# Performance work log

Measured on AMD Instinct MI355X. Metric: run time of the kernel, lower is better.

## Reference

```python
import jax, jax.numpy as jnp
import numpy as np

N = 50000
E = 800000
IN_DIM = 128
HID = 128
HEADS = 8
OUT_DIM = 64
NEG_SLOPE = 0.2


def setup_inputs() -> dict:
    key = jax.random.key(0)
    ks = jax.random.split(key, 10)
    x = jax.random.normal(ks[0], (N, IN_DIM), dtype=jnp.float32)
    edge_index = jax.random.randint(ks[1], (2, E), 0, N, dtype=jnp.int64)
    c1 = HID // HEADS  # 16 per-head channels, layer 1
    # layer 1 params (GATConv: lin has no bias; att_src/att_dst are [1,H,C])
    W1 = jax.random.normal(ks[2], (IN_DIM, HEADS * c1), dtype=jnp.float32) * 0.1
    att_src1 = jax.random.normal(ks[3], (1, HEADS, c1), dtype=jnp.float32) * 0.1
    att_dst1 = jax.random.normal(ks[4], (1, HEADS, c1), dtype=jnp.float32) * 0.1
    b1 = jnp.zeros((HEADS * c1,), dtype=jnp.float32)  # concat=True -> bias size H*C
    # layer 2 params (heads=1, concat=False)
    W2 = jax.random.normal(ks[5], (HID, OUT_DIM), dtype=jnp.float32) * 0.1
    att_src2 = jax.random.normal(ks[6], (1, 1, OUT_DIM), dtype=jnp.float32) * 0.1
    att_dst2 = jax.random.normal(ks[7], (1, 1, OUT_DIM), dtype=jnp.float32) * 0.1
    b2 = jnp.zeros((OUT_DIM,), dtype=jnp.float32)
    return {"x": x, "edge_index": edge_index,
            "W1": W1, "att_src1": att_src1, "att_dst1": att_dst1, "b1": b1,
            "W2": W2, "att_src2": att_src2, "att_dst2": att_dst2, "b2": b2}


def _gat_conv(x, src, dst, W, att_src, att_dst, bias, heads, concat):
    n = x.shape[0]
    c = W.shape[1] // heads
    h = (x @ W).reshape(n, heads, c)                      # [N,H,C]
    a_src = jnp.sum(h * att_src, axis=-1)                 # [N,H]
    a_dst = jnp.sum(h * att_dst, axis=-1)                 # [N,H]
    e = a_src[src] + a_dst[dst]                           # [E,H]
    e = jnp.where(e > 0, e, NEG_SLOPE * e)                # leaky_relu
    # segment softmax over incoming edges of each dst node
    m = jax.ops.segment_max(e, dst, num_segments=n)       # [N,H]
    ex = jnp.exp(e - m[dst])
    denom = jax.ops.segment_sum(ex, dst, num_segments=n)  # [N,H]
    alpha = ex / (denom[dst] + 1e-16)                     # [E,H]
    msg = h[src] * alpha[:, :, None]                      # [E,H,C]
    out = jax.ops.segment_sum(msg, dst, num_segments=n)   # [N,H,C]
    out = out.reshape(n, heads * c) if concat else out.mean(axis=1)
    return out + bias


def reference(x, edge_index, W1, att_src1, att_dst1, b1, W2, att_src2, att_dst2, b2):
    # add self-loops (PyG GATConv default add_self_loops=True)
    loops = jnp.arange(N, dtype=edge_index.dtype)
    src = jnp.concatenate([edge_index[0], loops])
    dst = jnp.concatenate([edge_index[1], loops])
    h = _gat_conv(x, src, dst, W1, att_src1, att_dst1, b1, HEADS, True)
    h = jax.nn.elu(h)
    out = _gat_conv(h, src, dst, W2, att_src2, att_dst2, b2, 1, False)
    return jax.nn.log_softmax(out, axis=1)
```

## Files before the change

kernel.cpp:

```cpp
#include <hip/hip_runtime.h>
#include <math.h>

#define N_NODES 50000
#define E_EDGES 800000
#define ET      (E_EDGES + N_NODES)
#define IN_DIM  128
#define HID     128
#define HEADS   8
#define C1      16
#define OUT_DIM 64
#define NEG_SLOPE 0.2f
#define LOG2E   1.4426950408889634f

#define TILE    8192
#define NT      ((ET + TILE - 1) / TILE)
#define NB      ((N_NODES + 255) / 256)

#define CONV_BLOCKS (N_NODES * IN_DIM / 4 / 256)
#define PREP_BLOCKS 112
#define MEGA_A (NT + CONV_BLOCKS + PREP_BLOCKS)
#define L1T_BLOCKS ((N_NODES + 63) / 64)
#define L1TA 391
#define L1TB (L1T_BLOCKS - L1TA)
#define FUSE_BLOCKS ((N_NODES + 15) / 16)

typedef unsigned int uint32;
typedef __attribute__((ext_vector_type(8))) short bf16x8;
typedef __attribute__((ext_vector_type(4))) float f32x4;
typedef __attribute__((ext_vector_type(2))) float f32x2;

static __device__ __forceinline__ unsigned short f2bf(float f) {
    uint32 u = __float_as_uint(f);
    u += 0x7FFFu + ((u >> 16) & 1u);
    return (unsigned short)(u >> 16);
}

static __device__ __forceinline__ unsigned char f2fp8(float f) {
    int pk = __builtin_amdgcn_cvt_pk_fp8_f32(f, f, 0, false);
    return (unsigned char)(pk & 0xFF);
}


__global__ __launch_bounds__(256) void prep_all(
        const int* __restrict__ dst, int* __restrict__ cnt,
        const float* __restrict__ x, unsigned short* __restrict__ xb,
        const float* __restrict__ W1, const float* __restrict__ as1,
        const float* __restrict__ ad1, const float* __restrict__ W2,
        const float* __restrict__ as2, const float* __restrict__ ad2,
        unsigned short* __restrict__ w1t, unsigned short* __restrict__ p1t,
        unsigned short* __restrict__ w2t, unsigned short* __restrict__ p2t) {
    __shared__ int hist[NB];
    int blk = blockIdx.x, t = threadIdx.x;
    if (blk < NT) {
        for (int b = t; b < NB; b += 256) hist[b] = 0;
        __syncthreads();
        int base = blk * TILE;
        #pragma unroll
        for (int it = 0; it < TILE / 256; ++it) {
            int i = base + it * 256 + t;
            if (i < ET) {
                int d = (i < E_EDGES) ? dst[i] : (i - E_EDGES);
                atomicAdd(&hist[d >> 8], 1);
            }
        }
        __syncthreads();
        for (int b = t; b < NB; b += 256) cnt[blk * NB + b] = hist[b];
    } else if (blk < NT + CONV_BLOCKS) {
        int i = (blk - NT) * 256 + t;
        float4 v = ((const float4*)x)[i];
        ushort4 o;
        o.x = f2bf(v.x); o.y = f2bf(v.y); o.z = f2bf(v.z); o.w = f2bf(v.w);
        ((ushort4*)xb)[i] = o;
    } else {
        int b = blk - NT - CONV_BLOCKS;
        if (b < 64) {
            int i = b * 256 + t;
            int n = i >> 7, k = i & 127;
            w1t[n * IN_DIM + k] = f2bf(W1[k * HID + n]);
        } else if (b < 96) {
            int i = (b - 64) * 256 + t;
            int n = i >> 7, k = i & 127;
            w2t[n * HID + k] = f2bf(W2[k * OUT_DIM + n]);
        } else if (b < 104) {
            int i = (b - 96) * 256 + t;
            int j = i >> 7, k = i & 127;
            int hh = j & 7;
            const float* a = (j < 8) ? as1 : ad1;
            float acc = 0.f;
            #pragma unroll
            for (int c = 0; c < C1; ++c)
                acc = fmaf(W1[k * HID + hh * C1 + c], a[hh * C1 + c], acc);
            p1t[j * IN_DIM + k] = f2bf(acc * LOG2E);
        } else {
            int i = (b - 104) * 256 + t;
            int j = i >> 7, k = i & 127;
            if (j < 2) {
                const float* a = (j == 0) ? as2 : ad2;
                float acc = 0.f;
                #pragma unroll
                for (int c = 0; c < OUT_DIM; ++c)
                    acc = fmaf(W2[k * OUT_DIM + c], a[c], acc);
                p2t[j * HID + k] = f2bf(acc * LOG2E);
            } else {
                p2t[j * HID + k] = 0;
            }
        }
    }
}


static __device__ __forceinline__ void l1_transform_body(
        int bb, int t,
        const unsigned short* __restrict__ xb, const unsigned short* __restrict__ w1t,
        const unsigned short* __restrict__ p1t, unsigned char* __restrict__ h1f,
        float* __restrict__ a_src, float* __restrict__ a_dst) {
    int w = t >> 6, lane = t & 63;
    int l15 = lane & 15, quad = lane >> 4;
    int n0 = bb * 64 + w * 16;
    int mrow = n0 + l15;
    int mload = (mrow < N_NODES) ? mrow : (N_NODES - 1);

    bf16x8 af[4];
    #pragma unroll
    for (int s = 0; s < 4; ++s)
        af[s] = *(const bf16x8*)&xb[(size_t)mload * IN_DIM + s * 32 + quad * 8];

    #pragma unroll
    for (int tt = 0; tt < 9; ++tt) {
        const unsigned short* Brow = (tt < 8) ? &w1t[(tt * 16 + l15) * IN_DIM]
                                              : &p1t[l15 * IN_DIM];
        f32x4 acc = {0.f, 0.f, 0.f, 0.f};
        #pragma unroll
        for (int s = 0; s < 4; ++s) {
            bf16x8 bf = *(const bf16x8*)&Brow[s * 32 + quad * 8];
            acc = __builtin_amdgcn_mfma_f32_16x16x32_bf16(af[s], bf, acc, 0, 0, 0);
        }
        int nodeb = n0 + quad * 4;
        if (tt < 8) {
            int ch = tt * 16 + l15;
            #pragma unroll
            for (int r = 0; r < 4; ++r)
                if (nodeb + r < N_NODES)
                    h1f[(size_t)(nodeb + r) * HID + ch] = f2fp8(acc[r]);
        } else {
            #pragma unroll
            for (int r = 0; r < 4; ++r) {
                if (nodeb + r < N_NODES) {
                    if (l15 < 8) a_src[(nodeb + r) * HEADS + l15] = acc[r];
                    else         a_dst[(nodeb + r) * HEADS + (l15 - 8)] = acc[r];
                }
            }
        }
    }
}


__global__ __launch_bounds__(256) void scatter_l1ta(
        const int* __restrict__ src, const int* __restrict__ dst,
        const int* __restrict__ cnt, int* __restrict__ bucketStart,
        uint32* __restrict__ pairs,
        const unsigned short* __restrict__ xb, const unsigned short* __restrict__ w1t,
        const unsigned short* __restrict__ p1t, unsigned char* __restrict__ h1f,
        float* __restrict__ a_src, float* __restrict__ a_dst) {
    __shared__ int lcur[NB];
    __shared__ int sscan[256];
    int t = threadIdx.x;
    if (blockIdx.x >= NT) {
        l1_transform_body(blockIdx.x - NT, t, xb, w1t, p1t, h1f, a_src, a_dst);
        return;
    }
    int tile = blockIdx.x;

    int run = 0, total = 0;
    if (t < NB) {
        for (int k = 0; k < NT; ++k) {
            int c = cnt[k * NB + t];
            if (k < tile) run += c;
            total += c;
        }
    }
    sscan[t] = (t < NB) ? total : 0;
    __syncthreads();
    #pragma unroll
    for (int off = 1; off < 256; off <<= 1) {
        int add = (t >= off) ? sscan[t - off] : 0;
        __syncthreads();
        sscan[t] += add;
        __syncthreads();
    }
    int bstart = sscan[t] - total;
    if (t < NB) {
        lcur[t] = bstart + run;
        if (tile == 0) bucketStart[t] = bstart;
    }
    if (tile == 0 && t == 0) bucketStart[NB] = ET;
    __syncthreads();

    int base = tile * TILE;
    #pragma unroll
    for (int it = 0; it < TILE / 256; ++it) {
        int i = base + it * 256 + t;
        if (i < ET) {
            int s, d;
            if (i < E_EDGES) { s = src[i]; d = dst[i]; }
            else             { s = d = i - E_EDGES; }
            int pos = atomicAdd(&lcur[d >> 8], 1);
            pairs[pos] = ((uint32)s << 8) | (uint32)(d & 255);
        }
    }
}


__global__ __launch_bounds__(256) void bucket_l1tb(
        const uint32* __restrict__ pairs, const int* __restrict__ bucketStart,
        int* __restrict__ row_start, int* __restrict__ csr_src,
        const unsigned short* __restrict__ xb, const unsigned short* __restrict__ w1t,
        const unsigned short* __restrict__ p1t, unsigned char* __restrict__ h1f,
        float* __restrict__ a_src, float* __restrict__ a_dst) {
    __shared__ int sdeg[256];
    __shared__ int sscan[256];
    int t = threadIdx.x;
    if (blockIdx.x >= NB) {
        l1_transform_body(blockIdx.x - NB + L1TA, t, xb, w1t, p1t, h1f, a_src, a_dst);
        return;
    }
    int b = blockIdx.x;
    int beg = bucketStart[b], end = bucketStart[b + 1];
    sdeg[t] = 0;
    __syncthreads();
    for (int j = beg + t; j < end; j += 256)
        atomicAdd(&sdeg[pairs[j] & 255u], 1);
    __syncthreads();
    int v = sdeg[t];
    sscan[t] = v;
    __syncthreads();
    #pragma unroll
    for (int off = 1; off < 256; off <<= 1) {
        int add = (t >= off) ? sscan[t - off] : 0;
        __syncthreads();
        sscan[t] += add;
        __syncthreads();
    }
    int pos0 = beg + sscan[t] - v;
    int n = b * 256 + t;
    if (n < N_NODES) row_start[n] = pos0;
    if (b == 0 && t == 0) row_start[N_NODES] = ET;
    __syncthreads();
    sscan[t] = pos0;
    __syncthreads();
    for (int j = beg + t; j < end; j += 256) {
        uint32 p = pairs[j];
        int pos = atomicAdd(&sscan[p & 255u], 1);
        csr_src[pos] = (int)(p >> 8);
    }
}


__global__ __launch_bounds__(256) void l1agg_l2t(
        const unsigned char* __restrict__ h1f, const float* __restrict__ a_src,
        const float* __restrict__ a_dst, const int* __restrict__ row_start,
        const int* __restrict__ csr_src, const float* __restrict__ b1,
        const unsigned short* __restrict__ w2t, const unsigned short* __restrict__ p2t,
        unsigned char* __restrict__ h2f, float* __restrict__ a_src2,
        float* __restrict__ a_dst2) {
    __shared__ unsigned short ha[16][128];
    __shared__ int sdeg16[16];
    __shared__ unsigned char perm[16];
    int t = threadIdx.x;
    int w = t >> 6;
    uint32 lane = t & 63;
    uint32 quarter = lane >> 4;
    uint32 lane16 = lane & 15;
    int n0blk = blockIdx.x * 16;

    if (t < 16) {
        int n = n0blk + t;
        int nc = (n < N_NODES) ? n : (N_NODES - 1);
        sdeg16[t] = row_start[nc + 1] - row_start[nc];
    }
    __syncthreads();
    if (t < 16) {
        int d = sdeg16[t];
        int r = 0;
        #pragma unroll
        for (int j = 0; j < 16; ++j) {
            int dj = sdeg16[j];
            r += (dj < d) || (dj == d && j < t);
        }
        perm[r] = (unsigned char)t;
    }
    __syncthreads();

    {
        uint32 c0 = lane16 * 8u;
        uint32 h = lane16 >> 1;
        int n_local = (int)perm[w * 4 + (int)quarter];
        int n = n0blk + n_local;
        int nc = (n < N_NODES) ? n : (N_NODES - 1);
        int beg = row_start[nc], end = row_start[nc + 1];
        int cnt = end - beg;
        int kmax = cnt;
        kmax = max(kmax, __shfl_xor(kmax, 16, 64));
        kmax = max(kmax, __shfl_xor(kmax, 32, 64));
        float adst = a_dst[nc * HEADS + h];
        float l = 0.f;
        float a0 = 0.f, a1 = 0.f, a2 = 0.f, a3 = 0.f;
        float a4 = 0.f, a5 = 0.f, a6 = 0.f, a7 = 0.f;

        auto edge = [&](float e0, uint2 u0, bool live) {
            float e = e0 + adst;
            e = fmaxf(e, NEG_SLOPE * e);
            e = live ? e : -10000.f;
            float p = exp2f(e);
            l += p;
            f32x2 f01 = __builtin_amdgcn_cvt_pk_f32_fp8((int)u0.x, false);
            f32x2 f23 = __builtin_amdgcn_cvt_pk_f32_fp8((int)u0.x, true);
            f32x2 f45 = __builtin_amdgcn_cvt_pk_f32_fp8((int)u0.y, false);
            f32x2 f67 = __builtin_amdgcn_cvt_pk_f32_fp8((int)u0.y, true);
            a0 = fmaf(p, f01[0], a0);
            a1 = fmaf(p, f01[1], a1);
            a2 = fmaf(p, f23[0], a2);
            a3 = fmaf(p, f23[1], a3);
            a4 = fmaf(p, f45[0], a4);
            a5 = fmaf(p, f45[1], a5);
            a6 = fmaf(p, f67[0], a6);
            a7 = fmaf(p, f67[1], a7);
        };

        int k = 0;
        uint32 ssn[8];
        if (k + 8 <= kmax) {
            #pragma unroll
            for (int q = 0; q < 8; ++q) {
                int j = beg + q;
                int jc = (j < end) ? j : (end - 1);
                ssn[q] = (uint32)csr_src[jc];
            }
        }
        for (; k + 8 <= kmax; k += 8) {
            uint32 ss[8]; float ee[8]; uint2 uu[8];
            #pragma unroll
            for (int q = 0; q < 8; ++q) ss[q] = ssn[q];
            #pragma unroll
            for (int q = 0; q < 8; ++q) ee[q] = a_src[ss[q] * 8u + h];
            #pragma unroll
            for (int q = 0; q < 8; ++q) uu[q] = *(const uint2*)&h1f[(ss[q] << 7) + c0];
            int kn = k + 8;
            if (kn + 8 <= kmax) {
                #pragma unroll
                for (int q = 0; q < 8; ++q) {
                    int j = beg + kn + q;
                    int jc = (j < end) ? j : (end - 1);
                    ssn[q] = (uint32)csr_src[jc];
                }
            }
            #pragma unroll
            for (int q = 0; q < 8; ++q) edge(ee[q], uu[q], k + q < cnt);
        }
        for (; k < kmax; k += 4) {
            uint32 ss[4]; float ee[4]; uint2 uu[4];
            #pragma unroll
            for (int q = 0; q < 4; ++q) {
                int j = beg + k + q;
                int jc = (j < end) ? j : (end - 1);
                ss[q] = (uint32)csr_src[jc];
            }
            #pragma unroll
            for (int q = 0; q < 4; ++q) ee[q] = a_src[ss[q] * 8u + h];
            #pragma unroll
            for (int q = 0; q < 4; ++q) uu[q] = *(const uint2*)&h1f[(ss[q] << 7) + c0];
            #pragma unroll
            for (int q = 0; q < 4; ++q) edge(ee[q], uu[q], k + q < cnt);
        }

        float inv = 1.f / (l + 1e-16f);
        float v0 = a0 * inv + b1[c0 + 0];
        float v1 = a1 * inv + b1[c0 + 1];
        float v2 = a2 * inv + b1[c0 + 2];
        float v3 = a3 * inv + b1[c0 + 3];
        float v4 = a4 * inv + b1[c0 + 4];
        float v5 = a5 * inv + b1[c0 + 5];
        float v6 = a6 * inv + b1[c0 + 6];
        float v7 = a7 * inv + b1[c0 + 7];
        v0 = v0 > 0.f ? v0 : (__expf(v0) - 1.f);
        v1 = v1 > 0.f ? v1 : (__expf(v1) - 1.f);
        v2 = v2 > 0.f ? v2 : (__expf(v2) - 1.f);
        v3 = v3 > 0.f ? v3 : (__expf(v3) - 1.f);
        v4 = v4 > 0.f ? v4 : (__expf(v4) - 1.f);
        v5 = v5 > 0.f ? v5 : (__expf(v5) - 1.f);
        v6 = v6 > 0.f ? v6 : (__expf(v6) - 1.f);
        v7 = v7 > 0.f ? v7 : (__expf(v7) - 1.f);
        uint4 packed;
        packed.x = (uint32)f2bf(v0) | ((uint32)f2bf(v1) << 16);
        packed.y = (uint32)f2bf(v2) | ((uint32)f2bf(v3) << 16);
        packed.z = (uint32)f2bf(v4) | ((uint32)f2bf(v5) << 16);
        packed.w = (uint32)f2bf(v6) | ((uint32)f2bf(v7) << 16);
        uint32 g = lane16 ^ ((uint32)n_local & 15u);
        *(uint4*)&ha[n_local][g * 8] = packed;
    }
    __syncthreads();

    {
        int l15 = (int)lane16, quad = (int)quarter;
        int n0 = n0blk;
        int nloc = l15;

        bf16x8 af[4];
        #pragma unroll
        for (int s = 0; s < 4; ++s) {
            uint32 g = (uint32)(s * 4 + quad) ^ (uint32)l15;
            af[s] = *(const bf16x8*)&ha[nloc][g * 8];
        }

        #pragma unroll
        for (int pass = 0; pass < 2; ++pass) {
            if (pass == 1 && w != 0) break;
            int tt = (pass == 0) ? w : 4;
            const unsigned short* Brow = (tt < 4) ? &w2t[(tt * 16 + l15) * HID]
                                                  : &p2t[l15 * HID];
            f32x4 acc = {0.f, 0.f, 0.f, 0.f};
            #pragma unroll
            for (int s = 0; s < 4; ++s) {
                bf16x8 bf = *(const bf16x8*)&Brow[s * 32 + quad * 8];
                acc = __builtin_amdgcn_mfma_f32_16x16x32_bf16(af[s], bf, acc, 0, 0, 0);
            }
            int nodeb = n0 + quad * 4;
            if (tt < 4) {
                int ch = tt * 16 + l15;
                #pragma unroll
                for (int r = 0; r < 4; ++r)
                    if (nodeb + r < N_NODES)
                        h2f[(size_t)(nodeb + r) * OUT_DIM + ch] = f2fp8(acc[r]);
            } else {
                #pragma unroll
                for (int r = 0; r < 4; ++r) {
                    if (nodeb + r < N_NODES) {
                        if (l15 == 0) a_src2[nodeb + r] = acc[r];
                        else if (l15 == 1) a_dst2[nodeb + r] = acc[r];
                    }
                }
            }
        }
    }
}


__global__ __launch_bounds__(256) void l2_aggregate(
        const unsigned char* __restrict__ h2f, const float* __restrict__ a_src2,
        const float* __restrict__ a_dst2, const int* __restrict__ row_start,
        const int* __restrict__ csr_src, const float* __restrict__ b2,
        float* __restrict__ out) {
    __shared__ int sdeg16[16];
    __shared__ int perm16[16];
    int t = threadIdx.x;
    int w = t >> 6;
    uint32 lane = t & 63;
    uint32 quarter = lane >> 4;
    uint32 lane16 = lane & 15;
    int nbase = blockIdx.x * 16;
    if (t < 16)
        sdeg16[t] = row_start[nbase + t + 1] - row_start[nbase + t];
    __syncthreads();
    if (t < 16) {
        int d = sdeg16[t];
        int r = 0;
        #pragma unroll
        for (int j = 0; j < 16; ++j) {
            int dj = sdeg16[j];
            r += (dj < d) || (dj == d && j < t);
        }
        perm16[r] = t;
    }
    __syncthreads();
    int n = nbase + perm16[w * 4 + (int)quarter];
    uint32 c0 = lane16 * 4u;
    int beg = row_start[n], end = row_start[n + 1];
    int cnt = end - beg;
    int kmax = cnt;
    kmax = max(kmax, __shfl_xor(kmax, 16, 64));
    kmax = max(kmax, __shfl_xor(kmax, 32, 64));
    float adst = a_dst2[n];
    float l = 0.f, a0 = 0.f, a1 = 0.f, a2 = 0.f, a3 = 0.f;

    auto edge2 = [&](float e0, uint32 u0, bool live) {
        float e = e0 + adst;
        e = fmaxf(e, NEG_SLOPE * e);
        e = live ? e : -10000.f;
        float p = exp2f(e);
        l += p;
        f32x2 f01 = __builtin_amdgcn_cvt_pk_f32_fp8((int)u0, false);
        f32x2 f23 = __builtin_amdgcn_cvt_pk_f32_fp8((int)u0, true);
        a0 = fmaf(p, f01[0], a0);
        a1 = fmaf(p, f01[1], a1);
        a2 = fmaf(p, f23[0], a2);
        a3 = fmaf(p, f23[1], a3);
    };

    int k = 0;
    uint32 ssn[8];
    if (k + 8 <= kmax) {
        #pragma unroll
        for (int q = 0; q < 8; ++q) {
            int j = beg + q;
            int jc = (j < end) ? j : (end - 1);
            ssn[q] = (uint32)csr_src[jc];
        }
    }
    for (; k + 8 <= kmax; k += 8) {
        uint32 ss[8]; float ee[8]; uint32 uu[8];
        #pragma unroll
        for (int q = 0; q < 8; ++q) ss[q] = ssn[q];
        #pragma unroll
        for (int q = 0; q < 8; ++q) ee[q] = a_src2[ss[q]];
        #pragma unroll
        for (int q = 0; q < 8; ++q) uu[q] = *(const uint32*)&h2f[(ss[q] << 6) + c0];
        int kn = k + 8;
        if (kn + 8 <= kmax) {
            #pragma unroll
            for (int q = 0; q < 8; ++q) {
                int j = beg + kn + q;
                int jc = (j < end) ? j : (end - 1);
                ssn[q] = (uint32)csr_src[jc];
            }
        }
        #pragma unroll
        for (int q = 0; q < 8; ++q) edge2(ee[q], uu[q], k + q < cnt);
    }
    for (; k < kmax; k += 4) {
        uint32 ss[4]; float ee[4]; uint32 uu[4];
        #pragma unroll
        for (int q = 0; q < 4; ++q) {
            int j = beg + k + q;
            int jc = (j < end) ? j : (end - 1);
            ss[q] = (uint32)csr_src[jc];
        }
        #pragma unroll
        for (int q = 0; q < 4; ++q) ee[q] = a_src2[ss[q]];
        #pragma unroll
        for (int q = 0; q < 4; ++q) uu[q] = *(const uint32*)&h2f[(ss[q] << 6) + c0];
        #pragma unroll
        for (int q = 0; q < 4; ++q) edge2(ee[q], uu[q], k + q < cnt);
    }

    float inv = 1.f / (l + 1e-16f);
    float o0 = a0 * inv + b2[c0 + 0];
    float o1 = a1 * inv + b2[c0 + 1];
    float o2 = a2 * inv + b2[c0 + 2];
    float o3 = a3 * inv + b2[c0 + 3];
    float mx = fmaxf(fmaxf(o0, o1), fmaxf(o2, o3));
    #pragma unroll
    for (int m = 8; m > 0; m >>= 1) mx = fmaxf(mx, __shfl_xor(mx, m, 16));
    float ex = __expf(o0 - mx) + __expf(o1 - mx) + __expf(o2 - mx) + __expf(o3 - mx);
    #pragma unroll
    for (int m = 8; m > 0; m >>= 1) ex += __shfl_xor(ex, m, 16);
    float lse = mx + __logf(ex);
    float4 o = make_float4(o0 - lse, o1 - lse, o2 - lse, o3 - lse);
    *(float4*)&out[(size_t)n * OUT_DIM + c0] = o;
}


extern "C" void kernel_launch(void* const* d_in, const int* in_sizes, int n_in,
                              void* d_out, int out_size, void* d_ws, size_t ws_size,
                              hipStream_t stream) {
    const float* x   = (const float*)d_in[0];
    const int*   ei  = (const int*)d_in[1];
    const float* W1  = (const float*)d_in[2];
    const float* as1 = (const float*)d_in[3];
    const float* ad1 = (const float*)d_in[4];
    const float* b1  = (const float*)d_in[5];
    const float* W2  = (const float*)d_in[6];
    const float* as2 = (const float*)d_in[7];
    const float* ad2 = (const float*)d_in[8];
    const float* b2  = (const float*)d_in[9];
    float* out = (float*)d_out;

    const int* src = ei;
    const int* dst = ei + E_EDGES;

    char* ws = (char*)d_ws;
    size_t off = 0;
    auto alloc = [&](size_t bytes) -> void* {
        void* p = ws + off;
        off += (bytes + 255) & ~size_t(255);
        return p;
    };
    unsigned short* xb     = (unsigned short*)alloc((size_t)N_NODES * IN_DIM * 2);
    unsigned char*  h1f    = (unsigned char*)alloc((size_t)N_NODES * HID);
    unsigned char*  h2f    = (unsigned char*)alloc((size_t)N_NODES * OUT_DIM);
    unsigned short* w1t    = (unsigned short*)alloc((size_t)HID * IN_DIM * 2);
    unsigned short* p1t    = (unsigned short*)alloc((size_t)16 * IN_DIM * 2);
    unsigned short* w2t    = (unsigned short*)alloc((size_t)OUT_DIM * HID * 2);
    unsigned short* p2t    = (unsigned short*)alloc((size_t)16 * HID * 2);
    float* a_src1    = (float*)alloc((size_t)N_NODES * HEADS * 4);
    float* a_dst1    = (float*)alloc((size_t)N_NODES * HEADS * 4);
    float* a_src2    = (float*)alloc((size_t)N_NODES * 4);
    float* a_dst2    = (float*)alloc((size_t)N_NODES * 4);
    int*   row_start = (int*)alloc((size_t)(N_NODES + 1) * 4);
    int*   csr_src   = (int*)alloc((size_t)ET * 4);
    uint32* pairs    = (uint32*)alloc((size_t)ET * 4);
    int*   cnt       = (int*)alloc((size_t)NB * NT * 4);
    int*   bucketStart = (int*)alloc((size_t)(NB + 1) * 4);

    prep_all<<<MEGA_A, 256, 0, stream>>>(dst, cnt, x, xb, W1, as1, ad1,
                                         W2, as2, ad2, w1t, p1t, w2t, p2t);
    scatter_l1ta<<<NT + L1TA, 256, 0, stream>>>(src, dst, cnt, bucketStart, pairs,
                                                xb, w1t, p1t, h1f, a_src1, a_dst1);
    bucket_l1tb<<<NB + L1TB, 256, 0, stream>>>(pairs, bucketStart, row_start, csr_src,
                                               xb, w1t, p1t, h1f, a_src1, a_dst1);
    l1agg_l2t<<<FUSE_BLOCKS, 256, 0, stream>>>(h1f, a_src1, a_dst1, row_start, csr_src,
                                               b1, w2t, p2t, h2f, a_src2, a_dst2);
    l2_aggregate<<<FUSE_BLOCKS, 256, 0, stream>>>(h2f, a_src2, a_dst2, row_start,
                                                  csr_src, b2, out);
}
```

Before: 187.8 us.

## Fuse x bf16 conversion into MFMA transform and double-buffer aggregation gathers

Removes the separate fp32-to-bf16 conversion of x in prep_all. The layer-1 transform now reads fp32 x directly and converts it in registers, which saves writing and re-reading a 12.8 MB bf16 copy. Both aggregation kernels also gain a deeper software pipeline: the gathered a_src and feature values for the next 8 edges load while the current 8 are processed. This hides gather latency at the cost of more registers and possibly lower occupancy.

```diff
diff --git a/kernel.cpp b/kernel.cpp
--- a/kernel.cpp
+++ b/kernel.cpp
@@ -16,9 +16,8 @@
 #define NT      ((ET + TILE - 1) / TILE)
 #define NB      ((N_NODES + 255) / 256)
 
-#define CONV_BLOCKS (N_NODES * IN_DIM / 4 / 256)
 #define PREP_BLOCKS 112
-#define MEGA_A (NT + CONV_BLOCKS + PREP_BLOCKS)
+#define MEGA_A (NT + PREP_BLOCKS)
 #define L1T_BLOCKS ((N_NODES + 63) / 64)
 #define L1TA 391
 #define L1TB (L1T_BLOCKS - L1TA)
@@ -43,7 +42,6 @@
 
 __global__ __launch_bounds__(256) void prep_all(
         const int* __restrict__ dst, int* __restrict__ cnt,
-        const float* __restrict__ x, unsigned short* __restrict__ xb,
         const float* __restrict__ W1, const float* __restrict__ as1,
         const float* __restrict__ ad1, const float* __restrict__ W2,
         const float* __restrict__ as2, const float* __restrict__ ad2,
@@ -65,14 +63,8 @@
         }
         __syncthreads();
         for (int b = t; b < NB; b += 256) cnt[blk * NB + b] = hist[b];
-    } else if (blk < NT + CONV_BLOCKS) {
-        int i = (blk - NT) * 256 + t;
-        float4 v = ((const float4*)x)[i];
-        ushort4 o;
-        o.x = f2bf(v.x); o.y = f2bf(v.y); o.z = f2bf(v.z); o.w = f2bf(v.w);
-        ((ushort4*)xb)[i] = o;
     } else {
-        int b = blk - NT - CONV_BLOCKS;
+        int b = blk - NT;
         if (b < 64) {
             int i = b * 256 + t;
             int n = i >> 7, k = i & 127;
@@ -111,7 +103,7 @@
 
 static __device__ __forceinline__ void l1_transform_body(
         int bb, int t,
-        const unsigned short* __restrict__ xb, const unsigned short* __restrict__ w1t,
+        const float* __restrict__ x, const unsigned short* __restrict__ w1t,
         const unsigned short* __restrict__ p1t, unsigned char* __restrict__ h1f,
         float* __restrict__ a_src, float* __restrict__ a_dst) {
     int w = t >> 6, lane = t & 63;
@@ -122,8 +114,17 @@
 
     bf16x8 af[4];
     #pragma unroll
-    for (int s = 0; s < 4; ++s)
-        af[s] = *(const bf16x8*)&xb[(size_t)mload * IN_DIM + s * 32 + quad * 8];
+    for (int s = 0; s < 4; ++s) {
+        const float* xr = &x[(size_t)mload * IN_DIM + s * 32 + quad * 8];
+        float4 lo = *(const float4*)xr;
+        float4 hi = *(const float4*)(xr + 4);
+        bf16x8 v;
+        v[0] = (short)f2bf(lo.x); v[1] = (short)f2bf(lo.y);
+        v[2] = (short)f2bf(lo.z); v[3] = (short)f2bf(lo.w);
+        v[4] = (short)f2bf(hi.x); v[5] = (short)f2bf(hi.y);
+        v[6] = (short)f2bf(hi.z); v[7] = (short)f2bf(hi.w);
+        af[s] = v;
+    }
 
     #pragma unroll
     for (int tt = 0; tt < 9; ++tt) {
@@ -159,14 +160,14 @@
         const int* __restrict__ src, const int* __restrict__ dst,
         const int* __restrict__ cnt, int* __restrict__ bucketStart,
         uint32* __restrict__ pairs,
-        const unsigned short* __restrict__ xb, const unsigned short* __restrict__ w1t,
+        const float* __restrict__ x, const unsigned short* __restrict__ w1t,
         const unsigned short* __restrict__ p1t, unsigned char* __restrict__ h1f,
         float* __restrict__ a_src, float* __restrict__ a_dst) {
     __shared__ int lcur[NB];
     __shared__ int sscan[256];
     int t = threadIdx.x;
     if (blockIdx.x >= NT) {
-        l1_transform_body(blockIdx.x - NT, t, xb, w1t, p1t, h1f, a_src, a_dst);
+        l1_transform_body(blockIdx.x - NT, t, x, w1t, p1t, h1f, a_src, a_dst);
         return;
     }
     int tile = blockIdx.x;
@@ -214,14 +215,14 @@
 __global__ __launch_bounds__(256) void bucket_l1tb(
         const uint32* __restrict__ pairs, const int* __restrict__ bucketStart,
         int* __restrict__ row_start, int* __restrict__ csr_src,
-        const unsigned short* __restrict__ xb, const unsigned short* __restrict__ w1t,
+        const float* __restrict__ x, const unsigned short* __restrict__ w1t,
         const unsigned short* __restrict__ p1t, unsigned char* __restrict__ h1f,
         float* __restrict__ a_src, float* __restrict__ a_dst) {
     __shared__ int sdeg[256];
     __shared__ int sscan[256];
     int t = threadIdx.x;
     if (blockIdx.x >= NB) {
-        l1_transform_body(blockIdx.x - NB + L1TA, t, xb, w1t, p1t, h1f, a_src, a_dst);
+        l1_transform_body(blockIdx.x - NB + L1TA, t, x, w1t, p1t, h1f, a_src, a_dst);
         return;
     }
     int b = blockIdx.x;
@@ -328,34 +329,50 @@
         };
 
         int k = 0;
-        uint32 ssn[8];
-        if (k + 8 <= kmax) {
+        uint32 ssN[8]; float eeA[8]; uint2 uuA[8];
+        if (kmax >= 8) {
             #pragma unroll
             for (int q = 0; q < 8; ++q) {
                 int j = beg + q;
                 int jc = (j < end) ? j : (end - 1);
-                ssn[q] = (uint32)csr_src[jc];
-            }
-        }
-        for (; k + 8 <= kmax; k += 8) {
-            uint32 ss[8]; float ee[8]; uint2 uu[8];
-            #pragma unroll
-            for (int q = 0; q < 8; ++q) ss[q] = ssn[q];
-            #pragma unroll
-            for (int q = 0; q < 8; ++q) ee[q] = a_src[ss[q] * 8u + h];
-            #pragma unroll
-            for (int q = 0; q < 8; ++q) uu[q] = *(const uint2*)&h1f[(ss[q] << 7) + c0];
-            int kn = k + 8;
-            if (kn + 8 <= kmax) {
+                ssN[q] = (uint32)csr_src[jc];
+            }
+            #pragma unroll
+            for (int q = 0; q < 8; ++q) eeA[q] = a_src[ssN[q] * 8u + h];
+            #pragma unroll
+            for (int q = 0; q < 8; ++q) uuA[q] = *(const uint2*)&h1f[(ssN[q] << 7) + c0];
+            if (kmax >= 16) {
                 #pragma unroll
                 for (int q = 0; q < 8; ++q) {
-                    int j = beg + kn + q;
+                    int j = beg + 8 + q;
                     int jc = (j < end) ? j : (end - 1);
-                    ssn[q] = (uint32)csr_src[jc];
+                    ssN[q] = (uint32)csr_src[jc];
                 }
             }
-            #pragma unroll
-            for (int q = 0; q < 8; ++q) edge(ee[q], uu[q], k + q < cnt);
+        }
+        for (; k + 16 <= kmax; k += 8) {
+            float eeB[8]; uint2 uuB[8];
+            #pragma unroll
+            for (int q = 0; q < 8; ++q) eeB[q] = a_src[ssN[q] * 8u + h];
+            #pragma unroll
+            for (int q = 0; q < 8; ++q) uuB[q] = *(const uint2*)&h1f[(ssN[q] << 7) + c0];
+            if (k + 24 <= kmax) {
+                #pragma unroll
+                for (int q = 0; q < 8; ++q) {
+                    int j = beg + k + 16 + q;
+                    int jc = (j < end) ? j : (end - 1);
+                    ssN[q] = (uint32)csr_src[jc];
+                }
+            }
+            #pragma unroll
+            for (int q = 0; q < 8; ++q) edge(eeA[q], uuA[q], k + q < cnt);
+            #pragma unroll
+            for (int q = 0; q < 8; ++q) { eeA[q] = eeB[q]; uuA[q] = uuB[q]; }
+        }
+        if (k + 8 <= kmax) {
+            #pragma unroll
+            for (int q = 0; q < 8; ++q) edge(eeA[q], uuA[q], k + q < cnt);
+            k += 8;
         }
         for (; k < kmax; k += 4) {
             uint32 ss[4]; float ee[4]; uint2 uu[4];
@@ -497,34 +514,50 @@
     };
 
     int k = 0;
-    uint32 ssn[8];
-    if (k + 8 <= kmax) {
+    uint32 ssN[8]; float eeA[8]; uint32 uuA[8];
+    if (kmax >= 8) {
         #pragma unroll
         for (int q = 0; q < 8; ++q) {
             int j = beg + q;
             int jc = (j < end) ? j : (end - 1);
-            ssn[q] = (uint32)csr_src[jc];
-        }
-    }
-    for (; k + 8 <= kmax; k += 8) {
-        uint32 ss[8]; float ee[8]; uint32 uu[8];
-        #pragma unroll
-        for (int q = 0; q < 8; ++q) ss[q] = ssn[q];
-        #pragma unroll
-        for (int q = 0; q < 8; ++q) ee[q] = a_src2[ss[q]];
-        #pragma unroll
-        for (int q = 0; q < 8; ++q) uu[q] = *(const uint32*)&h2f[(ss[q] << 6) + c0];
-        int kn = k + 8;
-        if (kn + 8 <= kmax) {
+            ssN[q] = (uint32)csr_src[jc];
+        }
+        #pragma unroll
+        for (int q = 0; q < 8; ++q) eeA[q] = a_src2[ssN[q]];
+        #pragma unroll
+        for (int q = 0; q < 8; ++q) uuA[q] = *(const uint32*)&h2f[(ssN[q] << 6) + c0];
+        if (kmax >= 16) {
             #pragma unroll
             for (int q = 0; q < 8; ++q) {
-                int j = beg + kn + q;
+                int j = beg + 8 + q;
                 int jc = (j < end) ? j : (end - 1);
-                ssn[q] = (uint32)csr_src[jc];
-            }
-        }
-        #pragma unroll
-        for (int q = 0; q < 8; ++q) edge2(ee[q], uu[q], k + q < cnt);
+                ssN[q] = (uint32)csr_src[jc];
+            }
+        }
+    }
+    for (; k + 16 <= kmax; k += 8) {
+        float eeB[8]; uint32 uuB[8];
+        #pragma unroll
+        for (int q = 0; q < 8; ++q) eeB[q] = a_src2[ssN[q]];
+        #pragma unroll
+        for (int q = 0; q < 8; ++q) uuB[q] = *(const uint32*)&h2f[(ssN[q] << 6) + c0];
+        if (k + 24 <= kmax) {
+            #pragma unroll
+            for (int q = 0; q < 8; ++q) {
+                int j = beg + k + 16 + q;
+                int jc = (j < end) ? j : (end - 1);
+                ssN[q] = (uint32)csr_src[jc];
+            }
+        }
+        #pragma unroll
+        for (int q = 0; q < 8; ++q) edge2(eeA[q], uuA[q], k + q < cnt);
+        #pragma unroll
+        for (int q = 0; q < 8; ++q) { eeA[q] = eeB[q]; uuA[q] = uuB[q]; }
+    }
+    if (k + 8 <= kmax) {
+        #pragma unroll
+        for (int q = 0; q < 8; ++q) edge2(eeA[q], uuA[q], k + q < cnt);
+        k += 8;
     }
     for (; k < kmax; k += 4) {
         uint32 ss[4]; float ee[4]; uint32 uu[4];
@@ -584,7 +617,6 @@
         off += (bytes + 255) & ~size_t(255);
         return p;
     };
-    unsigned short* xb     = (unsigned short*)alloc((size_t)N_NODES * IN_DIM * 2);
     unsigned char*  h1f    = (unsigned char*)alloc((size_t)N_NODES * HID);
     unsigned char*  h2f    = (unsigned char*)alloc((size_t)N_NODES * OUT_DIM);
     unsigned short* w1t    = (unsigned short*)alloc((size_t)HID * IN_DIM * 2);
@@ -601,12 +633,12 @@
     int*   cnt       = (int*)alloc((size_t)NB * NT * 4);
     int*   bucketStart = (int*)alloc((size_t)(NB + 1) * 4);
 
-    prep_all<<<MEGA_A, 256, 0, stream>>>(dst, cnt, x, xb, W1, as1, ad1,
+    prep_all<<<MEGA_A, 256, 0, stream>>>(dst, cnt, W1, as1, ad1,
                                          W2, as2, ad2, w1t, p1t, w2t, p2t);
     scatter_l1ta<<<NT + L1TA, 256, 0, stream>>>(src, dst, cnt, bucketStart, pairs,
-                                                xb, w1t, p1t, h1f, a_src1, a_dst1);
+                                                x, w1t, p1t, h1f, a_src1, a_dst1);
     bucket_l1tb<<<NB + L1TB, 256, 0, stream>>>(pairs, bucketStart, row_start, csr_src,
-                                               xb, w1t, p1t, h1f, a_src1, a_dst1);
+                                               x, w1t, p1t, h1f, a_src1, a_dst1);
     l1agg_l2t<<<FUSE_BLOCKS, 256, 0, stream>>>(h1f, a_src1, a_dst1, row_start, csr_src,
                                                b1, w2t, p2t, h2f, a_src2, a_dst2);
     l2_aggregate<<<FUSE_BLOCKS, 256, 0, stream>>>(h2f, a_src2, a_dst2, row_start,
```

After: 191.0 us. No clear change (+1.7%).
